# Performance work log

Hardware: AMD Instinct MI355X
Metric: run time of the kernel (lower is better)

## Reference

```python
import jax, jax.numpy as jnp
import numpy as np

B, T, N, L, D, F = 8, 1024, 512, 4096, 512, 64  # batch, target, nodes, leaves, d_model, d_feature
BR = L // N  # branching factor: leaves per node


def setup_inputs() -> dict:
    key = jax.random.key(0)
    ks = jax.random.split(key, 10)
    s = 0.02
    return {
        "root": jax.random.normal(ks[0], (B, 1, F), dtype=jnp.float32),
        "node": jax.random.normal(ks[1], (B, N, D), dtype=jnp.float32),
        "leaf": jax.random.normal(ks[2], (B, L, D), dtype=jnp.float32),
        "target": jax.random.normal(ks[3], (B, T, D), dtype=jnp.float32),
        "Wq": jax.random.normal(ks[4], (D, F), dtype=jnp.float32) * s,
        "bq": jnp.zeros((F,), dtype=jnp.float32),
        "Wk": jax.random.normal(ks[5], (D, F), dtype=jnp.float32) * s,
        "bk": jnp.zeros((F,), dtype=jnp.float32),
        "Wv": jax.random.normal(ks[6], (D, F), dtype=jnp.float32) * s,
        "bv": jnp.zeros((F,), dtype=jnp.float32),
        "Wagg": jax.random.normal(ks[7], (D, 1), dtype=jnp.float32) * s,
        "bagg": jnp.zeros((1,), dtype=jnp.float32),
    }


def reference(root, node, leaf, target, Wq, bq, Wk, bk, Wv, bv, Wagg, bagg):
    # Shared DecoderLinear projections (same weights used for node and leaf).
    q = target @ Wq + bq                      # [B,T,F]
    node_k = node @ Wk + bk                   # [B,N,F]
    node_v = node @ Wv + bv                   # [B,N,F]
    leaf_k = leaf @ Wk + bk                   # [B,L,F]
    leaf_v = leaf @ Wv + bv                   # [B,L,F]

    scale = 1.0 / jnp.sqrt(jnp.asarray(F, dtype=q.dtype))
    # Dual-key attention weights (no value-matmul inside attention()).
    Aqn = jax.nn.softmax(jnp.einsum('btf,bnf->btn', q, node_k) * scale, axis=-1)  # [B,T,N]
    Aql = jax.nn.softmax(jnp.einsum('btf,blf->btl', q, leaf_k) * scale, axis=-1)  # [B,T,L]

    # Tree interpolation: each leaf mixes root, its parent node value, and itself.
    node_rep = jnp.repeat(node_v, BR, axis=1)               # [B,L,F]
    interp = (root + node_rep + leaf_v) / 3.0               # [B,L,F]

    # Upward cumulative aggregation: suffix mean along the leaf dimension.
    rev_cumsum = jnp.cumsum(interp[:, ::-1, :], axis=1)[:, ::-1, :]  # [B,L,F]
    counts = (L - jnp.arange(L)).astype(interp.dtype)[None, :, None]
    upward = rev_cumsum / counts                                     # [B,L,F]

    # Weighted aggregation: learned softmax weights over each node's leaf group.
    w = jax.nn.softmax((leaf @ Wagg + bagg).reshape(B, N, BR), axis=-1)   # [B,N,BR]
    node_hat = jnp.einsum('bnc,bncf->bnf', w, upward.reshape(B, N, BR, F))  # [B,N,F]

    # Fused cat + matmul + softmax.
    A = jnp.concatenate([Aqn, Aql], axis=-1)          # [B,T,N+L]
    V = jnp.concatenate([node_hat, leaf_v], axis=-2)  # [B,N+L,F]
    return jax.nn.softmax(jnp.einsum('btm,bmf->btf', A, V), axis=-1)  # [B,T,F]
```

## Files before the change

### kernel.cpp

```cpp
#include <hip/hip_runtime.h>

#define B_ 8
#define T_ 1024
#define N_ 512
#define L_ 4096
#define D_ 512
#define F_ 64
#define SLICES 8
#define TPS 9
#define KSTR 72
#define XSTR 520

typedef __attribute__((ext_vector_type(8))) short short8;
typedef __attribute__((ext_vector_type(4))) float f32x4;

__device__ __forceinline__ unsigned short f2bf(float x){
    unsigned u = __builtin_bit_cast(unsigned, x);
    u += 0x7FFFu + ((u >> 16) & 1u);
    return (unsigned short)(u >> 16);
}
__device__ __forceinline__ unsigned pack_bf(float lo, float hi){
    return (unsigned)f2bf(lo) | ((unsigned)f2bf(hi) << 16);
}
__device__ __forceinline__ float bf2f(unsigned short s){
    return __builtin_bit_cast(float, ((unsigned)s) << 16);
}
__device__ __forceinline__ short8 frag_from4(unsigned d0, unsigned d1, unsigned d2, unsigned d3){
    union { unsigned u[4]; short8 s; } t;
    t.u[0] = d0; t.u[1] = d1; t.u[2] = d2; t.u[3] = d3;
    return t.s;
}

__global__ __launch_bounds__(64)
void prep_kernel(const float* __restrict__ Wq, const float* __restrict__ bq,
                 const float* __restrict__ Wk, const float* __restrict__ bk,
                 const float* __restrict__ Wv, const float* __restrict__ bv,
                 unsigned short* __restrict__ Wq_t, unsigned short* __restrict__ Wkv_t,
                 float* __restrict__ bq_s, float* __restrict__ bkv)
{
    const int n = blockIdx.x;
    const int lane = threadIdx.x;
    if (n == 192) {
        bq_s[lane]   = bq[lane] * 0.125f;
        bkv[lane]    = bk[lane];
        bkv[64+lane] = bv[lane];
        return;
    }
    const int d0 = lane * 8;
    unsigned short t[8];
    if (n < 64) {
        #pragma unroll
        for (int j = 0; j < 8; ++j) t[j] = f2bf(Wq[(size_t)(d0+j)*F_ + n] * 0.125f);
        *(uint4*)&Wq_t[(size_t)n*D_ + d0] = make_uint4(
            (unsigned)t[0]|((unsigned)t[1]<<16), (unsigned)t[2]|((unsigned)t[3]<<16),
            (unsigned)t[4]|((unsigned)t[5]<<16), (unsigned)t[6]|((unsigned)t[7]<<16));
    } else {
        const int nn  = n - 64;
        const float* W = (nn < 64) ? Wk : Wv;
        const int col = nn & 63;
        #pragma unroll
        for (int j = 0; j < 8; ++j) t[j] = f2bf(W[(size_t)(d0+j)*F_ + col]);
        *(uint4*)&Wkv_t[(size_t)nn*D_ + d0] = make_uint4(
            (unsigned)t[0]|((unsigned)t[1]<<16), (unsigned)t[2]|((unsigned)t[3]<<16),
            (unsigned)t[4]|((unsigned)t[5]<<16), (unsigned)t[6]|((unsigned)t[7]<<16));
    }
}

template<int MODE>
__device__ __forceinline__ void proj_body(
    int r0, unsigned short* Xs, unsigned short* Ws, unsigned short* Vt_lds,
    const float* __restrict__ X,
    const unsigned short* __restrict__ Wt,
    const float* __restrict__ bias,
    const float* __restrict__ Wagg, const float* __restrict__ bagg,
    unsigned short* __restrict__ outK, float* __restrict__ outVf,
    unsigned short* __restrict__ outVt, float* __restrict__ outAgg)
{
    constexpr int NPASS = (MODE == 0) ? 1 : 2;
    const int tid = threadIdx.x;
    const int w = tid >> 6, l = tid & 63, c = l & 15, h = l >> 4;

    const float4* xsrc = (const float4*)(X + (size_t)r0 * D_);
    #pragma unroll 4
    for (int j = 0; j < 32; ++j) {
        const int s = tid + j * 256;
        const float4 v = xsrc[s];
        *(uint2*)&Xs[(s >> 7)*XSTR + (s & 127)*4] =
            make_uint2(pack_bf(v.x, v.y), pack_bf(v.z, v.w));
    }
    {
        const int r = tid >> 2, ch = tid & 3;
        const unsigned short* src = Wt + (size_t)r * D_;
        #pragma unroll
        for (int j = 0; j < 16; ++j) {
            const int u = (ch + 4*j) * 8;
            *(uint4*)&Ws[r*XSTR + u] = *(const uint4*)(src + u);
        }
    }
    __syncthreads();

    #pragma unroll
    for (int p = 0; p < NPASS; ++p) {
        f32x4 acc[4];
        #pragma unroll
        for (int m = 0; m < 4; ++m) acc[m] = (f32x4){0,0,0,0};

        #pragma unroll
        for (int kk = 0; kk < 16; ++kk) {
            const short8 bfr = *(const short8*)&Ws[(16*w + c)*XSTR + kk*32 + 8*h];
            #pragma unroll
            for (int m = 0; m < 4; ++m) {
                const short8 af = *(const short8*)&Xs[(16*m + c)*XSTR + kk*32 + 8*h];
                acc[m] = __builtin_amdgcn_mfma_f32_16x16x32_bf16(af, bfr, acc[m], 0,0,0);
            }
        }

        const float bc = bias[64*p + 16*w + c];
        #pragma unroll
        for (int m = 0; m < 4; ++m) {
            #pragma unroll
            for (int r = 0; r < 4; ++r) {
                const int row = r0 + 16*m + 4*h + r;
                const float v = acc[m][r] + bc;
                if (MODE == 0 || p == 0) {
                    outK[(size_t)row*F_ + 16*w + c] = f2bf(v);
                } else if (MODE == 1) {
                    outVf[(size_t)row*F_ + 16*w + c] = v;
                } else {
                    Vt_lds[(16*w + c)*72 + 16*m + 4*h + r] = f2bf(v);
                }
            }
        }

        if (p + 1 < NPASS) {
            __syncthreads();
            const int r = tid >> 2, ch = tid & 3;
            const unsigned short* src = Wt + (size_t)(64 + r) * D_;
            #pragma unroll
            for (int j = 0; j < 16; ++j) {
                const int u = (ch + 4*j) * 8;
                *(uint4*)&Ws[r*XSTR + u] = *(const uint4*)(src + u);
            }
            __syncthreads();
        }
    }

    if constexpr (MODE == 2) {
        __syncthreads();
        {
            const int row = tid >> 2, qd = tid & 3;
            const unsigned short* xr = &Xs[row*XSTR + qd*128];
            const float* wr = Wagg + qd*128;
            float p = 0.f;
            #pragma unroll
            for (int j = 0; j < 16; ++j) {
                const short8 xv = *(const short8*)(xr + j*8);
                const float4 wa0 = *(const float4*)(wr + j*8);
                const float4 wa1 = *(const float4*)(wr + j*8 + 4);
                p += bf2f((unsigned short)xv[0])*wa0.x + bf2f((unsigned short)xv[1])*wa0.y
                   + bf2f((unsigned short)xv[2])*wa0.z + bf2f((unsigned short)xv[3])*wa0.w
                   + bf2f((unsigned short)xv[4])*wa1.x + bf2f((unsigned short)xv[5])*wa1.y
                   + bf2f((unsigned short)xv[6])*wa1.z + bf2f((unsigned short)xv[7])*wa1.w;
            }
            p += __shfl_xor(p, 1);
            p += __shfl_xor(p, 2);
            if (qd == 0) outAgg[r0 + row] = p + bagg[0];
        }
        {
            const int f = tid >> 2, seg = tid & 3;
            const int b = r0 >> 12, l0 = r0 & (L_ - 1);
            const uint4 a0 = *(const uint4*)&Vt_lds[f*72 + seg*16];
            const uint4 a1 = *(const uint4*)&Vt_lds[f*72 + seg*16 + 8];
            unsigned short* dst = outVt + ((size_t)(b*F_ + f))*L_ + l0 + seg*16;
            *(uint4*)dst = a0;
            *(uint4*)(dst + 8) = a1;
        }
    }
}

__global__ __launch_bounds__(256)
void proj_all(const float* __restrict__ target, const float* __restrict__ node,
              const float* __restrict__ leaf,
              const unsigned short* __restrict__ Wq_t,
              const unsigned short* __restrict__ Wkv_t,
              const float* __restrict__ bq_s, const float* __restrict__ bkv,
              const float* __restrict__ Wagg, const float* __restrict__ bagg,
              unsigned short* __restrict__ q_bf, unsigned short* __restrict__ nk_bf,
              float* __restrict__ node_v, unsigned short* __restrict__ lk_bf,
              unsigned short* __restrict__ lvt, float* __restrict__ agg)
{
    __shared__ unsigned short Xs[64 * XSTR];
    __shared__ unsigned short Ws[64 * XSTR];
    __shared__ unsigned short Vt_lds[64 * 72];
    const int blk = blockIdx.x;
    if (blk < 512) {
        proj_body<2>(blk*64, Xs, Ws, Vt_lds, leaf, Wkv_t, bkv, Wagg, bagg,
                     lk_bf, nullptr, lvt, agg);
    } else if (blk < 640) {
        proj_body<0>((blk-512)*64, Xs, Ws, Vt_lds, target, Wq_t, bq_s, nullptr, nullptr,
                     q_bf, nullptr, nullptr, nullptr);
    } else {
        proj_body<1>((blk-640)*64, Xs, Ws, Vt_lds, node, Wkv_t, bkv, nullptr, nullptr,
                     nk_bf, node_v, nullptr, nullptr);
    }
}

__global__ __launch_bounds__(256)
void scan_nh_kernel(const unsigned short* __restrict__ lvt,
                    const float* __restrict__ node_v,
                    const float* __restrict__ root,
                    const float* __restrict__ agg,
                    unsigned short* __restrict__ nh_t)
{
    const int gtid = blockIdx.x * 256 + threadIdx.x;
    const int wv   = gtid >> 6;
    const int lane = threadIdx.x & 63;
    const int b = wv >> 6;
    const int f = wv & 63;

    const unsigned short* vt = lvt + ((size_t)(b*F_ + f))*L_ + lane*64;
    const float rootf = root[b*F_ + f];
    short8 xv[8]; float nv[8]; float gv[8];
    #pragma unroll
    for (int g = 0; g < 8; ++g) {
        xv[g] = *(const short8*)(vt + g*8);
        nv[g] = node_v[((size_t)(b*N_ + lane*8 + g))*F_ + f];
        float s8 = 0.f;
        #pragma unroll
        for (int j = 0; j < 8; ++j) s8 += bf2f((unsigned short)xv[g][j]);
        gv[g] = (s8 + 8.f*(rootf + nv[g])) * (1.f/3.f);
    }

    float s[9];
    s[8] = 0.f;
    #pragma unroll
    for (int j = 7; j >= 0; --j) s[j] = s[j+1] + gv[j];

    float x = s[0];
    const float lsum = x;
    #pragma unroll
    for (int off = 1; off < 64; off <<= 1) {
        float t = __shfl_down(x, off);
        if (lane + off < 64) x += t;
    }
    const float excl = x - lsum;

    const float* aggb = agg + (size_t)b*L_ + lane*64;
    unsigned short out8[8];
    #pragma unroll
    for (int g = 0; g < 8; ++g) {
        const float4 a0 = *(const float4*)(aggb + g*8);
        const float4 a1 = *(const float4*)(aggb + g*8 + 4);
        const float av[8] = {a0.x,a0.y,a0.z,a0.w, a1.x,a1.y,a1.z,a1.w};
        float mx = av[0];
        #pragma unroll
        for (int cc = 1; cc < 8; ++cc) mx = fmaxf(mx, av[cc]);
        float wgt[8]; float wsum = 0.f;
        #pragma unroll
        for (int cc = 0; cc < 8; ++cc) { wgt[cc] = __expf(av[cc] - mx); wsum += wgt[cc]; }

        const float tn = excl + s[g+1];
        float run = 0.f, acc = 0.f;
        #pragma unroll
        for (int cc = 7; cc >= 0; --cc) {
            const int ll = lane*64 + g*8 + cc;
            const float interp = (rootf + nv[g] + bf2f((unsigned short)xv[g][cc])) * (1.f/3.f);
            run += interp;
            const float up = (tn + run) / (float)(L_ - ll);
            acc = fmaf(wgt[cc], up, acc);
        }
        out8[g] = f2bf(acc / wsum);
    }
    *(uint4*)&nh_t[((size_t)(b*F_ + f))*N_ + lane*8] = *(const uint4*)out8;
}

__global__ __launch_bounds__(512, 4)
void attn_kernel(const unsigned short* __restrict__ qb,
                 const unsigned short* __restrict__ nk,
                 const unsigned short* __restrict__ nht,
                 const unsigned short* __restrict__ lk,
                 const unsigned short* __restrict__ lvt,
                 unsigned short* __restrict__ pacc, float* __restrict__ pd)
{
    __shared__ unsigned short Ks[2][64*KSTR];
    __shared__ unsigned short Vt[2][64*KSTR];

    const int wg  = (blockIdx.x & 7) * 64 + (blockIdx.x >> 3);
    const int b   = wg >> 6;
    const int sl  = (wg >> 3) & 7;
    const int t0  = (wg & 7) * 128;

    const int tid = threadIdx.x;
    const int w   = tid >> 6;
    const int l   = tid & 63;
    const int c   = l & 15;
    const int h   = l >> 4;
    const int sm  = tid >> 3;
    const int sc  = tid & 7;

    const unsigned short* qrow = qb + ((size_t)(b*T_ + t0 + w*16 + c))*F_ + 8*h;
    const short8 qf0 = *(const short8*)qrow;
    const short8 qf1 = *(const short8*)(qrow + 32);

    f32x4 accN[4] = {{0,0,0,0},{0,0,0,0},{0,0,0,0},{0,0,0,0}};
    f32x4 accL[4] = {{0,0,0,0},{0,0,0,0},{0,0,0,0},{0,0,0,0}};
    float dsN = 0.f, dsL = 0.f;

    const unsigned short* Knb = nk  + (size_t)b*N_*F_;
    const unsigned short* Klb = lk  + (size_t)b*L_*F_;
    const unsigned short* Vnb = nht + (size_t)b*F_*N_;
    const unsigned short* Vlb = lvt + (size_t)b*F_*L_;

    const int ti0 = sl * TPS;

    uint4 sk0, sv0;
    auto load_tile = [&](int ti) {
        if (ti < 8) {
            sk0 = *(const uint4*)(Knb + (size_t)ti*64*F_ + sm*64 + sc*8);
            sv0 = *(const uint4*)(Vnb + (size_t)sm*N_ + ti*64 + sc*8);
        } else {
            sk0 = *(const uint4*)(Klb + (size_t)(ti-8)*64*F_ + sm*64 + sc*8);
            sv0 = *(const uint4*)(Vlb + (size_t)sm*L_ + (ti-8)*64 + sc*8);
        }
    };
    auto write_tile = [&](int pb) {
        *(uint4*)&Ks[pb][sm*KSTR + sc*8] = sk0;
        *(uint4*)&Vt[pb][sm*KSTR + sc*8] = sv0;
    };

    load_tile(ti0);
    write_tile(0);
    __syncthreads();

    const int srcA = c + 16*((2*h) & 3);
    const int srcB = c + 16*((2*h + 1) & 3);
    const int hs   = h >> 1;

    for (int i = 0; i < TPS; ++i) {
        const int  ti  = ti0 + i;
        const bool isN = ti < 8;
        const int  pb  = i & 1;
        const bool nxt = (i + 1 < TPS);
        if (nxt) load_tile(ti + 1);

        f32x4 st[4] = {{0,0,0,0},{0,0,0,0},{0,0,0,0},{0,0,0,0}};
        #pragma unroll
        for (int ss = 0; ss < 4; ++ss) {
            const short8 kf0 = *(const short8*)&Ks[pb][(16*ss + c)*KSTR + 8*h];
            st[ss] = __builtin_amdgcn_mfma_f32_16x16x32_bf16(kf0, qf0, st[ss], 0,0,0);
            const short8 kf1 = *(const short8*)&Ks[pb][(16*ss + c)*KSTR + 32 + 8*h];
            st[ss] = __builtin_amdgcn_mfma_f32_16x16x32_bf16(kf1, qf1, st[ss], 0,0,0);
        }

        unsigned pk0[4], pk1[4];
        float psum = 0.f;
        #pragma unroll
        for (int ss = 0; ss < 4; ++ss) {
            #pragma unroll
            for (int r = 0; r < 4; ++r) { st[ss][r] = __expf(st[ss][r]); psum += st[ss][r]; }
            pk0[ss] = pack_bf(st[ss][0], st[ss][1]);
            pk1[ss] = pack_bf(st[ss][2], st[ss][3]);
        }
        if (isN) dsN += psum; else dsL += psum;

        #pragma unroll
        for (int k00 = 0; k00 < 2; ++k00) {
            const unsigned d0a = __shfl(pk0[2*k00+0], srcA);
            const unsigned d0b = __shfl(pk0[2*k00+1], srcA);
            const unsigned d1a = __shfl(pk1[2*k00+0], srcA);
            const unsigned d1b = __shfl(pk1[2*k00+1], srcA);
            const unsigned d2a = __shfl(pk0[2*k00+0], srcB);
            const unsigned d2b = __shfl(pk0[2*k00+1], srcB);
            const unsigned d3a = __shfl(pk1[2*k00+0], srcB);
            const unsigned d3b = __shfl(pk1[2*k00+1], srcB);
            const short8 bp = frag_from4(hs ? d0b : d0a, hs ? d1b : d1a,
                                         hs ? d2b : d2a, hs ? d3b : d3a);
            if (isN) {
                #pragma unroll
                for (int s2 = 0; s2 < 4; ++s2) {
                    const short8 af = *(const short8*)&Vt[pb][(16*s2 + c)*KSTR + 32*k00 + 8*h];
                    accN[s2] = __builtin_amdgcn_mfma_f32_16x16x32_bf16(af, bp, accN[s2], 0,0,0);
                }
            } else {
                #pragma unroll
                for (int s2 = 0; s2 < 4; ++s2) {
                    const short8 af = *(const short8*)&Vt[pb][(16*s2 + c)*KSTR + 32*k00 + 8*h];
                    accL[s2] = __builtin_amdgcn_mfma_f32_16x16x32_bf16(af, bp, accL[s2], 0,0,0);
                }
            }
        }

        if (nxt) {
            write_tile(pb ^ 1);
            __syncthreads();
        }
    }

    dsN += __shfl_xor(dsN, 16);  dsN += __shfl_xor(dsN, 32);
    dsL += __shfl_xor(dsL, 16);  dsL += __shfl_xor(dsL, 32);

    const int gt = b*T_ + t0 + w*16 + c;
    unsigned short* baseN = pacc + (((size_t)sl*(B_*T_) + gt)*2 + 0)*F_;
    unsigned short* baseL = baseN + F_;
    #pragma unroll
    for (int s2 = 0; s2 < 4; ++s2) {
        *(unsigned*)&baseN[s2*16 + 4*h]     = pack_bf(accN[s2][0], accN[s2][1]);
        *(unsigned*)&baseN[s2*16 + 4*h + 2] = pack_bf(accN[s2][2], accN[s2][3]);
        *(unsigned*)&baseL[s2*16 + 4*h]     = pack_bf(accL[s2][0], accL[s2][1]);
        *(unsigned*)&baseL[s2*16 + 4*h + 2] = pack_bf(accL[s2][2], accL[s2][3]);
    }
    if (h == 0) {
        pd[((size_t)sl*(B_*T_) + gt)*2 + 0] = dsN;
        pd[((size_t)sl*(B_*T_) + gt)*2 + 1] = dsL;
    }
}

__global__ __launch_bounds__(256)
void combine_kernel(const unsigned short* __restrict__ pacc,
                    const float* __restrict__ pd,
                    float* __restrict__ out)
{
    const int gt = (blockIdx.x * 256 + threadIdx.x) >> 6;
    const int f  = threadIdx.x & 63;

    float aN = 0.f, aL = 0.f, dN = 0.f, dL = 0.f;
    #pragma unroll
    for (int s = 0; s < SLICES; ++s) {
        const size_t base = ((size_t)s*(B_*T_) + gt)*2;
        aN += bf2f(pacc[(base + 0)*F_ + f]);
        aL += bf2f(pacc[(base + 1)*F_ + f]);
        dN += pd[base + 0];
        dL += pd[base + 1];
    }
    float lg = aN / dN + aL / dL;
    float mx = lg;
    #pragma unroll
    for (int off = 1; off < 64; off <<= 1) mx = fmaxf(mx, __shfl_xor(mx, off));
    const float e = __expf(lg - mx);
    float ssum = e;
    #pragma unroll
    for (int off = 1; off < 64; off <<= 1) ssum += __shfl_xor(ssum, off);
    out[(size_t)gt*F_ + f] = e / ssum;
}

extern "C" void kernel_launch(void* const* d_in, const int* in_sizes, int n_in,
                              void* d_out, int out_size, void* d_ws, size_t ws_size,
                              hipStream_t stream)
{
    const float* root   = (const float*)d_in[0];
    const float* node   = (const float*)d_in[1];
    const float* leaf   = (const float*)d_in[2];
    const float* target = (const float*)d_in[3];
    const float* Wq   = (const float*)d_in[4];
    const float* bq   = (const float*)d_in[5];
    const float* Wk   = (const float*)d_in[6];
    const float* bk   = (const float*)d_in[7];
    const float* Wv   = (const float*)d_in[8];
    const float* bv   = (const float*)d_in[9];
    const float* Wagg = (const float*)d_in[10];
    const float* bagg = (const float*)d_in[11];
    float* out = (float*)d_out;

    char* wp = (char*)d_ws;
    unsigned short* q_bf  = (unsigned short*)wp; wp += (size_t)B_*T_*F_*2;
    unsigned short* nk_bf = (unsigned short*)wp; wp += (size_t)B_*N_*F_*2;
    unsigned short* lk_bf = (unsigned short*)wp; wp += (size_t)B_*L_*F_*2;
    unsigned short* lvt   = (unsigned short*)wp; wp += (size_t)B_*F_*L_*2;
    unsigned short* nht   = (unsigned short*)wp; wp += (size_t)B_*F_*N_*2;
    unsigned short* Wq_t  = (unsigned short*)wp; wp += (size_t)64*D_*2;
    unsigned short* Wkv_t = (unsigned short*)wp; wp += (size_t)128*D_*2;
    float* node_v = (float*)wp; wp += (size_t)B_*N_*F_*4;
    float* agg    = (float*)wp; wp += (size_t)B_*L_*4;
    float* bq_s   = (float*)wp; wp += 512;
    float* bkv    = (float*)wp; wp += 512;
    unsigned short* pacc = (unsigned short*)wp; wp += (size_t)SLICES*B_*T_*2*F_*2;
    float* pd     = (float*)wp;

    prep_kernel<<<193, 64, 0, stream>>>(Wq, bq, Wk, bk, Wv, bv, Wq_t, Wkv_t, bq_s, bkv);
    proj_all<<<704, 256, 0, stream>>>(target, node, leaf, Wq_t, Wkv_t, bq_s, bkv,
                                      Wagg, bagg, q_bf, nk_bf, node_v, lk_bf, lvt, agg);
    scan_nh_kernel<<<128, 256, 0, stream>>>(lvt, node_v, root, agg, nht);
    attn_kernel<<<B_*(T_/128)*SLICES, 512, 0, stream>>>(q_bf, nk_bf, nht, lk_bf, lvt, pacc, pd);
    combine_kernel<<<(B_*T_)/4, 256, 0, stream>>>(pacc, pd, out);
}
```

Before: 86.90 us.

## Use 1024 threads per projection block, one MFMA tile per wave

```diff
diff --git a/kernel.cpp b/kernel.cpp
--- a/kernel.cpp
+++ b/kernel.cpp
@@ -78,69 +78,59 @@
 {
     constexpr int NPASS = (MODE == 0) ? 1 : 2;
     const int tid = threadIdx.x;
-    const int w = tid >> 6, l = tid & 63, c = l & 15, h = l >> 4;
+    const int l = tid & 63, c = l & 15, h = l >> 4;
+    const int w  = tid >> 6;
+    const int nt = w & 3;
+    const int m  = w >> 2;
 
     const float4* xsrc = (const float4*)(X + (size_t)r0 * D_);
-    #pragma unroll 4
-    for (int j = 0; j < 32; ++j) {
-        const int s = tid + j * 256;
+    #pragma unroll
+    for (int j = 0; j < 8; ++j) {
+        const int s = tid + j * 1024;
         const float4 v = xsrc[s];
         *(uint2*)&Xs[(s >> 7)*XSTR + (s & 127)*4] =
             make_uint2(pack_bf(v.x, v.y), pack_bf(v.z, v.w));
     }
     {
-        const int r = tid >> 2, ch = tid & 3;
-        const unsigned short* src = Wt + (size_t)r * D_;
-        #pragma unroll
-        for (int j = 0; j < 16; ++j) {
-            const int u = (ch + 4*j) * 8;
-            *(uint4*)&Ws[r*XSTR + u] = *(const uint4*)(src + u);
-        }
+        const int r = tid >> 4, ch = tid & 15;
+        const unsigned short* src = Wt + (size_t)r * D_ + ch*8;
+        #pragma unroll
+        for (int j = 0; j < 4; ++j)
+            *(uint4*)&Ws[r*XSTR + ch*8 + j*128] = *(const uint4*)(src + j*128);
     }
     __syncthreads();
 
     #pragma unroll
     for (int p = 0; p < NPASS; ++p) {
-        f32x4 acc[4];
-        #pragma unroll
-        for (int m = 0; m < 4; ++m) acc[m] = (f32x4){0,0,0,0};
-
+        f32x4 acc = {0,0,0,0};
         #pragma unroll
         for (int kk = 0; kk < 16; ++kk) {
-            const short8 bfr = *(const short8*)&Ws[(16*w + c)*XSTR + kk*32 + 8*h];
-            #pragma unroll
-            for (int m = 0; m < 4; ++m) {
-                const short8 af = *(const short8*)&Xs[(16*m + c)*XSTR + kk*32 + 8*h];
-                acc[m] = __builtin_amdgcn_mfma_f32_16x16x32_bf16(af, bfr, acc[m], 0,0,0);
-            }
-        }
-
-        const float bc = bias[64*p + 16*w + c];
-        #pragma unroll
-        for (int m = 0; m < 4; ++m) {
-            #pragma unroll
-            for (int r = 0; r < 4; ++r) {
-                const int row = r0 + 16*m + 4*h + r;
-                const float v = acc[m][r] + bc;
-                if (MODE == 0 || p == 0) {
-                    outK[(size_t)row*F_ + 16*w + c] = f2bf(v);
-                } else if (MODE == 1) {
-                    outVf[(size_t)row*F_ + 16*w + c] = v;
-                } else {
-                    Vt_lds[(16*w + c)*72 + 16*m + 4*h + r] = f2bf(v);
-                }
+            const short8 bfr = *(const short8*)&Ws[(16*nt + c)*XSTR + kk*32 + 8*h];
+            const short8 af  = *(const short8*)&Xs[(16*m  + c)*XSTR + kk*32 + 8*h];
+            acc = __builtin_amdgcn_mfma_f32_16x16x32_bf16(af, bfr, acc, 0,0,0);
+        }
+
+        const float bc = bias[64*p + 16*nt + c];
+        #pragma unroll
+        for (int r = 0; r < 4; ++r) {
+            const int row = r0 + 16*m + 4*h + r;
+            const float v = acc[r] + bc;
+            if (MODE == 0 || p == 0) {
+                outK[(size_t)row*F_ + 16*nt + c] = f2bf(v);
+            } else if (MODE == 1) {
+                outVf[(size_t)row*F_ + 16*nt + c] = v;
+            } else {
+                Vt_lds[(16*nt + c)*72 + 16*m + 4*h + r] = f2bf(v);
             }
         }
 
         if (p + 1 < NPASS) {
             __syncthreads();
-            const int r = tid >> 2, ch = tid & 3;
-            const unsigned short* src = Wt + (size_t)(64 + r) * D_;
+            const int r = tid >> 4, ch = tid & 15;
+            const unsigned short* src = Wt + (size_t)(64 + r) * D_ + ch*8;
             #pragma unroll
-            for (int j = 0; j < 16; ++j) {
-                const int u = (ch + 4*j) * 8;
-                *(uint4*)&Ws[r*XSTR + u] = *(const uint4*)(src + u);
-            }
+            for (int j = 0; j < 4; ++j)
+                *(uint4*)&Ws[r*XSTR + ch*8 + j*128] = *(const uint4*)(src + j*128);
             __syncthreads();
         }
     }
@@ -148,37 +138,36 @@
     if constexpr (MODE == 2) {
         __syncthreads();
         {
-            const int row = tid >> 2, qd = tid & 3;
-            const unsigned short* xr = &Xs[row*XSTR + qd*128];
-            const float* wr = Wagg + qd*128;
-            float p = 0.f;
+            const int row = tid >> 4, qd = tid & 15;
+            const unsigned short* xr = &Xs[row*XSTR + qd*32];
+            const float* wr = Wagg + qd*32;
+            float pa = 0.f;
             #pragma unroll
-            for (int j = 0; j < 16; ++j) {
+            for (int j = 0; j < 4; ++j) {
                 const short8 xv = *(const short8*)(xr + j*8);
                 const float4 wa0 = *(const float4*)(wr + j*8);
                 const float4 wa1 = *(const float4*)(wr + j*8 + 4);
-                p += bf2f((unsigned short)xv[0])*wa0.x + bf2f((unsigned short)xv[1])*wa0.y
-                   + bf2f((unsigned short)xv[2])*wa0.z + bf2f((unsigned short)xv[3])*wa0.w
-                   + bf2f((unsigned short)xv[4])*wa1.x + bf2f((unsigned short)xv[5])*wa1.y
-                   + bf2f((unsigned short)xv[6])*wa1.z + bf2f((unsigned short)xv[7])*wa1.w;
+                pa += bf2f((unsigned short)xv[0])*wa0.x + bf2f((unsigned short)xv[1])*wa0.y
+                    + bf2f((unsigned short)xv[2])*wa0.z + bf2f((unsigned short)xv[3])*wa0.w
+                    + bf2f((unsigned short)xv[4])*wa1.x + bf2f((unsigned short)xv[5])*wa1.y
+                    + bf2f((unsigned short)xv[6])*wa1.z + bf2f((unsigned short)xv[7])*wa1.w;
             }
-            p += __shfl_xor(p, 1);
-            p += __shfl_xor(p, 2);
-            if (qd == 0) outAgg[r0 + row] = p + bagg[0];
+            pa += __shfl_xor(pa, 1);
+            pa += __shfl_xor(pa, 2);
+            pa += __shfl_xor(pa, 4);
+            pa += __shfl_xor(pa, 8);
+            if (qd == 0) outAgg[r0 + row] = pa + bagg[0];
         }
         {
-            const int f = tid >> 2, seg = tid & 3;
+            const int f = tid >> 4, seg = tid & 15;
             const int b = r0 >> 12, l0 = r0 & (L_ - 1);
-            const uint4 a0 = *(const uint4*)&Vt_lds[f*72 + seg*16];
-            const uint4 a1 = *(const uint4*)&Vt_lds[f*72 + seg*16 + 8];
-            unsigned short* dst = outVt + ((size_t)(b*F_ + f))*L_ + l0 + seg*16;
-            *(uint4*)dst = a0;
-            *(uint4*)(dst + 8) = a1;
-        }
-    }
-}
-
-__global__ __launch_bounds__(256)
+            const uint2 a0 = *(const uint2*)&Vt_lds[f*72 + seg*4];
+            *(uint2*)(outVt + ((size_t)(b*F_ + f))*L_ + l0 + seg*4) = a0;
+        }
+    }
+}
+
+__global__ __launch_bounds__(1024, 4)
 void proj_all(const float* __restrict__ target, const float* __restrict__ node,
               const float* __restrict__ leaf,
               const unsigned short* __restrict__ Wq_t,
@@ -477,8 +466,8 @@
     float* pd     = (float*)wp;
 
     prep_kernel<<<193, 64, 0, stream>>>(Wq, bq, Wk, bk, Wv, bv, Wq_t, Wkv_t, bq_s, bkv);
-    proj_all<<<704, 256, 0, stream>>>(target, node, leaf, Wq_t, Wkv_t, bq_s, bkv,
-                                      Wagg, bagg, q_bf, nk_bf, node_v, lk_bf, lvt, agg);
+    proj_all<<<704, 1024, 0, stream>>>(target, node, leaf, Wq_t, Wkv_t, bq_s, bkv,
+                                       Wagg, bagg, q_bf, nk_bf, node_v, lk_bf, lvt, agg);
     scan_nh_kernel<<<128, 256, 0, stream>>>(lvt, node_v, root, agg, nht);
     attn_kernel<<<B_*(T_/128)*SLICES, 512, 0, stream>>>(q_bf, nk_bf, nht, lk_bf, lvt, pacc, pd);
     combine_kernel<<<(B_*T_)/4, 256, 0, stream>>>(pacc, pd, out);
```

New measurement: 86.48 us. About the same (-0.5%).
